# Performance work log

Measured on AMD Instinct MI355X. Metric: run time of the kernel, lower is better.

## Reference

```python
import jax, jax.numpy as jnp
import numpy as np

N, K, D, H, O = 50000, 32, 128, 32, 128


def setup_inputs() -> dict:
    key = jax.random.key(0)
    ks = jax.random.split(key, 8)
    node_feats = jax.random.normal(ks[0], (N, D), dtype=jnp.float32)
    neib_feats = jax.random.normal(ks[1], (N * K, D), dtype=jnp.float32)
    node_ids = jax.random.randint(ks[2], (N,), 0, N)
    neib_ids = jax.random.randint(ks[3], (N * K,), 0, N)
    s = 1.0 / np.sqrt(D)
    W_att1 = jax.random.uniform(ks[4], (D, H), jnp.float32, -s, s)   # Linear(D,H,bias=False)
    sh = 1.0 / np.sqrt(H)
    W_att2 = jax.random.uniform(ks[5], (H, H), jnp.float32, -sh, sh)  # Linear(H,H,bias=False)
    W_node = jax.random.uniform(ks[6], (D, O), jnp.float32, -s, s)
    W_neib = jax.random.uniform(ks[7], (D, O), jnp.float32, -s, s)
    return {"node_feats": node_feats, "neib_feats": neib_feats,
            "node_ids": node_ids, "neib_ids": neib_ids,
            "W_att1": W_att1, "W_att2": W_att2,
            "W_node": W_node, "W_neib": W_neib}


def reference(node_feats, neib_feats, node_ids, neib_ids, W_att1, W_att2, W_node, W_neib):
    n = node_feats.shape[0]
    k = neib_feats.shape[0] // n
    att = lambda x: jnp.tanh(x @ W_att1) @ W_att2           # Linear->Tanh->Linear
    neib_att = att(neib_feats).reshape(n, k, -1)             # [N, K, H]
    node_att = att(node_feats)                               # [N, H]
    scores = jnp.einsum('nkh,nh->nk', neib_att, node_att)    # bmm + squeeze
    ws = jax.nn.softmax(scores, axis=-1)                     # [N, K]
    agg = jnp.einsum('nkd,nk->nd', neib_feats.reshape(n, k, -1), ws)  # weighted neighbor sum
    out = jnp.concatenate([node_feats @ W_node, agg @ W_neib], axis=1)
    return jax.nn.relu(out)
```

## Files before the change

### kernel.cpp

```cpp
#include <hip/hip_runtime.h>

#define N_NODES 50000
#define KNB 32
#define DIM 128
#define HDIM 32

typedef _Float16 f16x8 __attribute__((ext_vector_type(8)));
typedef float f32x16 __attribute__((ext_vector_type(16)));

__device__ __forceinline__ float fast_tanh(float x) {
  float xc = fminf(fmaxf(x, -15.f), 15.f);
  float e = __expf(2.f * xc);
  return (e - 1.f) / (e + 1.f);
}

__global__ __launch_bounds__(256) void k_att(
    const float* __restrict__ node_feats, const float* __restrict__ neib_feats,
    const float* __restrict__ W_att1, const float* __restrict__ W_att2,
    float* __restrict__ out) {
  __shared__ float w2p[HDIM * 33];
  __shared__ float s_tn[4][HDIM];
  __shared__ float s_na[4][HDIM];
  __shared__ float s_sc[4][KNB];

  const int tid = threadIdx.x;
  const int wv = tid >> 6;
  const int l = tid & 63;
  const int lg = l & 31;
  const int hf = l >> 5;

  for (int i = tid; i < HDIM * HDIM; i += 256)
    w2p[(i >> 5) * 33 + (i & 31)] = W_att2[i];

  f16x8 b1[8];
#pragma unroll
  for (int s = 0; s < 8; ++s) {
#pragma unroll
    for (int j = 0; j < 8; ++j) {
      int d = s * 16 + hf * 8 + j;
      b1[s][j] = (_Float16)W_att1[d * HDIM + lg];
    }
  }
  __syncthreads();

  const int waveG = blockIdx.x * 4 + wv;
  const int nW = gridDim.x * 4;
  const int iters = (N_NODES + nW - 1) / nW;

  for (int it = 0; it < iters; ++it) {
    const int n = waveG + it * nW;
    const bool active = n < N_NODES;
    const int nn = active ? n : N_NODES - 1;
    const float* nb = neib_feats + (size_t)nn * (KNB * DIM);
    const float* nd = node_feats + (size_t)nn * DIM;

    f32x16 acc = {0.f, 0.f, 0.f, 0.f, 0.f, 0.f, 0.f, 0.f,
                  0.f, 0.f, 0.f, 0.f, 0.f, 0.f, 0.f, 0.f};
    f32x16 acc2 = {0.f, 0.f, 0.f, 0.f, 0.f, 0.f, 0.f, 0.f,
                   0.f, 0.f, 0.f, 0.f, 0.f, 0.f, 0.f, 0.f};
#pragma unroll
    for (int s = 0; s < 8; ++s) {
      const float* srcA = nb + lg * DIM + s * 16 + hf * 8;
      const float* srcN = nd + s * 16 + hf * 8;
      f16x8 a, an;
#pragma unroll
      for (int j = 0; j < 8; ++j) {
        a[j] = (_Float16)srcA[j];
        an[j] = (_Float16)srcN[j];
      }
      acc = __builtin_amdgcn_mfma_f32_32x32x16_f16(a, b1[s], acc, 0, 0, 0);
      acc2 = __builtin_amdgcn_mfma_f32_32x32x16_f16(an, b1[s], acc2, 0, 0, 0);
    }

    float T[16];
#pragma unroll
    for (int r = 0; r < 16; ++r) T[r] = fast_tanh(acc[r]);

    float tn = fast_tanh(acc2[0]);
    if (l < 32) s_tn[wv][l] = tn;
    __syncthreads();

    float na = 0.f;
#pragma unroll
    for (int g = 0; g < HDIM; ++g) na = fmaf(s_tn[wv][g], w2p[g * 33 + lg], na);
    if (l < 32) s_na[wv][l] = na;
    __syncthreads();

    float v = 0.f;
#pragma unroll
    for (int h = 0; h < HDIM; ++h) v = fmaf(w2p[lg * 33 + h], s_na[wv][h], v);

#pragma unroll
    for (int r = 0; r < 16; ++r) {
      float p = T[r] * v;
#pragma unroll
      for (int off = 1; off <= 16; off <<= 1) p += __shfl_xor(p, off);
      if (lg == 0) s_sc[wv][(r & 3) + 8 * (r >> 2) + 4 * hf] = p;
    }
    __syncthreads();

    float sc = s_sc[wv][lg];
    float mx = sc;
#pragma unroll
    for (int off = 16; off; off >>= 1) mx = fmaxf(mx, __shfl_xor(mx, off));
    float e = __expf(sc - mx);
    float sum = e;
#pragma unroll
    for (int off = 16; off; off >>= 1) sum += __shfl_xor(sum, off);
    float w = e / sum;

    float a0 = 0.f, a1 = 0.f;
#pragma unroll 8
    for (int k = 0; k < KNB; ++k) {
      float wk = __shfl(w, k, 32);
      float2 rv = *(const float2*)(nb + k * DIM + 2 * l);
      a0 = fmaf(wk, rv.x, a0);
      a1 = fmaf(wk, rv.y, a1);
    }
    if (active)
      *(float2*)(out + (size_t)n * 256 + 128 + 2 * l) = make_float2(a0, a1);
  }
}

__global__ __launch_bounds__(256) void k_out(
    const float* __restrict__ node_feats, const float* __restrict__ W_node,
    const float* __restrict__ W_neib, float* __restrict__ out) {
  const int tid = threadIdx.x;
  const int wv = tid >> 6;
  const int l = tid & 63;
  const int lg = l & 31;
  const int hf = l >> 5;
  const int half = blockIdx.y;

  const float* W = half ? W_neib : W_node;
  const int r0 = blockIdx.x * 128 + wv * 32;
  const int row = r0 + lg;
  const int rowc = row < N_NODES ? row : N_NODES - 1;

  const float* X = half ? (out + 128) : node_feats;
  const size_t pitch = half ? 256 : DIM;

  f16x8 a[8];
#pragma unroll
  for (int s = 0; s < 8; ++s) {
    const float* src = X + (size_t)rowc * pitch + s * 16 + hf * 8;
#pragma unroll
    for (int j = 0; j < 8; ++j) a[s][j] = (_Float16)src[j];
  }

  for (int ct = 0; ct < 4; ++ct) {
    f32x16 acc = {0.f, 0.f, 0.f, 0.f, 0.f, 0.f, 0.f, 0.f,
                  0.f, 0.f, 0.f, 0.f, 0.f, 0.f, 0.f, 0.f};
#pragma unroll
    for (int s = 0; s < 8; ++s) {
      f16x8 b;
#pragma unroll
      for (int j = 0; j < 8; ++j) {
        int d = s * 16 + hf * 8 + j;
        b[j] = (_Float16)W[d * 128 + ct * 32 + lg];
      }
      acc = __builtin_amdgcn_mfma_f32_32x32x16_f16(a[s], b, acc, 0, 0, 0);
    }
#pragma unroll
    for (int r = 0; r < 16; ++r) {
      int orow = r0 + (r & 3) + 8 * (r >> 2) + 4 * hf;
      if (orow < N_NODES)
        out[(size_t)orow * 256 + half * 128 + ct * 32 + lg] = fmaxf(acc[r], 0.f);
    }
  }
}

extern "C" void kernel_launch(void* const* d_in, const int* in_sizes, int n_in,
                              void* d_out, int out_size, void* d_ws, size_t ws_size,
                              hipStream_t stream) {
  (void)in_sizes; (void)n_in; (void)d_ws; (void)ws_size; (void)out_size;
  const float* node_feats = (const float*)d_in[0];
  const float* neib_feats = (const float*)d_in[1];
  const float* W_att1 = (const float*)d_in[4];
  const float* W_att2 = (const float*)d_in[5];
  const float* W_node = (const float*)d_in[6];
  const float* W_neib = (const float*)d_in[7];
  float* out = (float*)d_out;

  k_att<<<dim3(768), dim3(256), 0, stream>>>(node_feats, neib_feats, W_att1, W_att2, out);
  k_out<<<dim3((N_NODES + 127) / 128, 2), dim3(256), 0, stream>>>(node_feats, W_node, W_neib, out);
}
```

Before: 1.246 ms.

## Precompute per-node attention query via W2·W2ᵀ and simplify neighbor scoring

After: 1.150 ms. -7.7%, faster.

```diff
diff --git a/kernel.cpp b/kernel.cpp
--- a/kernel.cpp
+++ b/kernel.cpp
@@ -9,105 +9,148 @@
 typedef float f32x16 __attribute__((ext_vector_type(16)));
 
 __device__ __forceinline__ float fast_tanh(float x) {
-  float xc = fminf(fmaxf(x, -15.f), 15.f);
+  float xc = fminf(fmaxf(x, -10.f), 10.f);
   float e = __expf(2.f * xc);
-  return (e - 1.f) / (e + 1.f);
-}
-
-__global__ __launch_bounds__(256) void k_att(
-    const float* __restrict__ node_feats, const float* __restrict__ neib_feats,
-    const float* __restrict__ W_att1, const float* __restrict__ W_att2,
-    float* __restrict__ out) {
-  __shared__ float w2p[HDIM * 33];
-  __shared__ float s_tn[4][HDIM];
-  __shared__ float s_na[4][HDIM];
-  __shared__ float s_sc[4][KNB];
+  return (e - 1.f) * __builtin_amdgcn_rcpf(e + 1.f);
+}
+
+__device__ __forceinline__ f32x16 zero16() {
+  f32x16 z;
+#pragma unroll
+  for (int i = 0; i < 16; ++i) z[i] = 0.f;
+  return z;
+}
+
+__global__ __launch_bounds__(256) void k_node(
+    const float* __restrict__ node_feats, const float* __restrict__ W_att1,
+    const float* __restrict__ W_att2, const float* __restrict__ W_node,
+    float* __restrict__ out, float* __restrict__ v_ws) {
+  __shared__ float w2s[HDIM * HDIM];
+  __shared__ float Ms[HDIM * 33];
+  __shared__ float T2[4][HDIM * 36];
 
   const int tid = threadIdx.x;
-  const int wv = tid >> 6;
-  const int l = tid & 63;
-  const int lg = l & 31;
-  const int hf = l >> 5;
-
-  for (int i = tid; i < HDIM * HDIM; i += 256)
-    w2p[(i >> 5) * 33 + (i & 31)] = W_att2[i];
-
-  f16x8 b1[8];
-#pragma unroll
-  for (int s = 0; s < 8; ++s) {
+  const int wv = tid >> 6, l = tid & 63, lg = l & 31, hf = l >> 5;
+
+  for (int i = tid; i < HDIM * HDIM; i += 256) w2s[i] = W_att2[i];
+  __syncthreads();
+  for (int e = tid; e < HDIM * HDIM; e += 256) {
+    int g = e >> 5, gp = e & 31;
+    float s = 0.f;
+#pragma unroll
+    for (int h = 0; h < HDIM; ++h) s = fmaf(w2s[g * 32 + h], w2s[gp * 32 + h], s);
+    Ms[g * 33 + gp] = s;
+  }
+  __syncthreads();
+
+  const int r0 = blockIdx.x * 128 + wv * 32;
+  const int row = r0 + lg;
+  const int rowc = row < N_NODES ? row : N_NODES - 1;
+
+  f16x8 af[8];
+#pragma unroll
+  for (int s = 0; s < 8; ++s) {
+    const float* src = node_feats + (size_t)rowc * DIM + s * 16 + hf * 8;
+#pragma unroll
+    for (int j = 0; j < 8; ++j) af[s][j] = (_Float16)src[j];
+  }
+
+  f32x16 acc1 = zero16();
+#pragma unroll
+  for (int s = 0; s < 8; ++s) {
+    f16x8 b;
+#pragma unroll
+    for (int j = 0; j < 8; ++j)
+      b[j] = (_Float16)W_att1[(s * 16 + hf * 8 + j) * HDIM + lg];
+    acc1 = __builtin_amdgcn_mfma_f32_32x32x16_f16(af[s], b, acc1, 0, 0, 0);
+  }
+#pragma unroll
+  for (int r = 0; r < 16; ++r)
+    T2[wv][((r & 3) + 8 * (r >> 2) + 4 * hf) * 36 + lg] = fast_tanh(acc1[r]);
+  __syncthreads();
+
+  f32x16 accv = zero16();
+#pragma unroll
+  for (int s = 0; s < 2; ++s) {
+    f16x8 a2, mb;
 #pragma unroll
     for (int j = 0; j < 8; ++j) {
-      int d = s * 16 + hf * 8 + j;
-      b1[s][j] = (_Float16)W_att1[d * HDIM + lg];
-    }
-  }
-  __syncthreads();
+      a2[j] = (_Float16)T2[wv][lg * 36 + s * 16 + hf * 8 + j];
+      mb[j] = (_Float16)Ms[(s * 16 + hf * 8 + j) * 33 + lg];
+    }
+    accv = __builtin_amdgcn_mfma_f32_32x32x16_f16(a2, mb, accv, 0, 0, 0);
+  }
+#pragma unroll
+  for (int r = 0; r < 16; ++r) {
+    int orow = r0 + (r & 3) + 8 * (r >> 2) + 4 * hf;
+    if (orow < N_NODES) v_ws[orow * HDIM + lg] = accv[r];
+  }
+
+  for (int ct = 0; ct < 4; ++ct) {
+    f32x16 acc = zero16();
+#pragma unroll
+    for (int s = 0; s < 8; ++s) {
+      f16x8 b;
+#pragma unroll
+      for (int j = 0; j < 8; ++j)
+        b[j] = (_Float16)W_node[(s * 16 + hf * 8 + j) * 128 + ct * 32 + lg];
+      acc = __builtin_amdgcn_mfma_f32_32x32x16_f16(af[s], b, acc, 0, 0, 0);
+    }
+#pragma unroll
+    for (int r = 0; r < 16; ++r) {
+      int orow = r0 + (r & 3) + 8 * (r >> 2) + 4 * hf;
+      if (orow < N_NODES) out[(size_t)orow * 256 + ct * 32 + lg] = fmaxf(acc[r], 0.f);
+    }
+  }
+}
+
+__global__ __launch_bounds__(256, 3) void k_att(
+    const float* __restrict__ neib_feats, const float* __restrict__ W_att1,
+    const float* __restrict__ v_ws, float* __restrict__ out) {
+  const int tid = threadIdx.x;
+  const int wv = tid >> 6, l = tid & 63, lg = l & 31, hf = l >> 5;
+
+  f16x8 w1t[8];
+#pragma unroll
+  for (int s = 0; s < 8; ++s) {
+#pragma unroll
+    for (int j = 0; j < 8; ++j)
+      w1t[s][j] = (_Float16)W_att1[(s * 16 + hf * 8 + j) * HDIM + lg];
+  }
 
   const int waveG = blockIdx.x * 4 + wv;
   const int nW = gridDim.x * 4;
-  const int iters = (N_NODES + nW - 1) / nW;
-
-  for (int it = 0; it < iters; ++it) {
-    const int n = waveG + it * nW;
-    const bool active = n < N_NODES;
-    const int nn = active ? n : N_NODES - 1;
-    const float* nb = neib_feats + (size_t)nn * (KNB * DIM);
-    const float* nd = node_feats + (size_t)nn * DIM;
-
-    f32x16 acc = {0.f, 0.f, 0.f, 0.f, 0.f, 0.f, 0.f, 0.f,
-                  0.f, 0.f, 0.f, 0.f, 0.f, 0.f, 0.f, 0.f};
-    f32x16 acc2 = {0.f, 0.f, 0.f, 0.f, 0.f, 0.f, 0.f, 0.f,
-                   0.f, 0.f, 0.f, 0.f, 0.f, 0.f, 0.f, 0.f};
+
+  for (int n = waveG; n < N_NODES; n += nW) {
+    const float* nb = neib_feats + (size_t)n * (KNB * DIM);
+
+    f32x16 acc = zero16();
 #pragma unroll
     for (int s = 0; s < 8; ++s) {
-      const float* srcA = nb + lg * DIM + s * 16 + hf * 8;
-      const float* srcN = nd + s * 16 + hf * 8;
-      f16x8 a, an;
-#pragma unroll
-      for (int j = 0; j < 8; ++j) {
-        a[j] = (_Float16)srcA[j];
-        an[j] = (_Float16)srcN[j];
-      }
-      acc = __builtin_amdgcn_mfma_f32_32x32x16_f16(a, b1[s], acc, 0, 0, 0);
-      acc2 = __builtin_amdgcn_mfma_f32_32x32x16_f16(an, b1[s], acc2, 0, 0, 0);
-    }
-
-    float T[16];
-#pragma unroll
-    for (int r = 0; r < 16; ++r) T[r] = fast_tanh(acc[r]);
-
-    float tn = fast_tanh(acc2[0]);
-    if (l < 32) s_tn[wv][l] = tn;
-    __syncthreads();
-
-    float na = 0.f;
-#pragma unroll
-    for (int g = 0; g < HDIM; ++g) na = fmaf(s_tn[wv][g], w2p[g * 33 + lg], na);
-    if (l < 32) s_na[wv][l] = na;
-    __syncthreads();
-
-    float v = 0.f;
-#pragma unroll
-    for (int h = 0; h < HDIM; ++h) v = fmaf(w2p[lg * 33 + h], s_na[wv][h], v);
-
+      const float* src = nb + lg * DIM + s * 16 + hf * 8;
+      f16x8 b;
+#pragma unroll
+      for (int j = 0; j < 8; ++j) b[j] = (_Float16)src[j];
+      acc = __builtin_amdgcn_mfma_f32_32x32x16_f16(w1t[s], b, acc, 0, 0, 0);
+    }
+
+    const float* vn = v_ws + n * HDIM;
+    float p = 0.f;
 #pragma unroll
     for (int r = 0; r < 16; ++r) {
-      float p = T[r] * v;
-#pragma unroll
-      for (int off = 1; off <= 16; off <<= 1) p += __shfl_xor(p, off);
-      if (lg == 0) s_sc[wv][(r & 3) + 8 * (r >> 2) + 4 * hf] = p;
-    }
-    __syncthreads();
-
-    float sc = s_sc[wv][lg];
-    float mx = sc;
-#pragma unroll
-    for (int off = 16; off; off >>= 1) mx = fmaxf(mx, __shfl_xor(mx, off));
-    float e = __expf(sc - mx);
+      float t = fast_tanh(acc[r]);
+      p = fmaf(t, vn[(r & 3) + 8 * (r >> 2) + 4 * hf], p);
+    }
+    p += __shfl_xor(p, 32, 64);
+
+    float mx = p;
+#pragma unroll
+    for (int off = 16; off; off >>= 1) mx = fmaxf(mx, __shfl_xor(mx, off, 32));
+    float e = __expf(p - mx);
     float sum = e;
 #pragma unroll
-    for (int off = 16; off; off >>= 1) sum += __shfl_xor(sum, off);
-    float w = e / sum;
+    for (int off = 16; off; off >>= 1) sum += __shfl_xor(sum, off, 32);
+    float w = e * __builtin_amdgcn_rcpf(sum);
 
     float a0 = 0.f, a1 = 0.f;
 #pragma unroll 8
@@ -117,55 +160,40 @@
       a0 = fmaf(wk, rv.x, a0);
       a1 = fmaf(wk, rv.y, a1);
     }
-    if (active)
-      *(float2*)(out + (size_t)n * 256 + 128 + 2 * l) = make_float2(a0, a1);
-  }
-}
-
-__global__ __launch_bounds__(256) void k_out(
-    const float* __restrict__ node_feats, const float* __restrict__ W_node,
+    *(float2*)(out + (size_t)n * 256 + 128 + 2 * l) = make_float2(a0, a1);
+  }
+}
+
+__global__ __launch_bounds__(256) void k_neib(
     const float* __restrict__ W_neib, float* __restrict__ out) {
   const int tid = threadIdx.x;
-  const int wv = tid >> 6;
-  const int l = tid & 63;
-  const int lg = l & 31;
-  const int hf = l >> 5;
-  const int half = blockIdx.y;
-
-  const float* W = half ? W_neib : W_node;
+  const int wv = tid >> 6, l = tid & 63, lg = l & 31, hf = l >> 5;
   const int r0 = blockIdx.x * 128 + wv * 32;
   const int row = r0 + lg;
   const int rowc = row < N_NODES ? row : N_NODES - 1;
 
-  const float* X = half ? (out + 128) : node_feats;
-  const size_t pitch = half ? 256 : DIM;
-
-  f16x8 a[8];
-#pragma unroll
-  for (int s = 0; s < 8; ++s) {
-    const float* src = X + (size_t)rowc * pitch + s * 16 + hf * 8;
-#pragma unroll
-    for (int j = 0; j < 8; ++j) a[s][j] = (_Float16)src[j];
+  f16x8 af[8];
+#pragma unroll
+  for (int s = 0; s < 8; ++s) {
+    const float* src = out + (size_t)rowc * 256 + 128 + s * 16 + hf * 8;
+#pragma unroll
+    for (int j = 0; j < 8; ++j) af[s][j] = (_Float16)src[j];
   }
 
   for (int ct = 0; ct < 4; ++ct) {
-    f32x16 acc = {0.f, 0.f, 0.f, 0.f, 0.f, 0.f, 0.f, 0.f,
-                  0.f, 0.f, 0.f, 0.f, 0.f, 0.f, 0.f, 0.f};
+    f32x16 acc = zero16();
 #pragma unroll
     for (int s = 0; s < 8; ++s) {
       f16x8 b;
 #pragma unroll
-      for (int j = 0; j < 8; ++j) {
-        int d = s * 16 + hf * 8 + j;
-        b[j] = (_Float16)W[d * 128 + ct * 32 + lg];
-      }
-      acc = __builtin_amdgcn_mfma_f32_32x32x16_f16(a[s], b, acc, 0, 0, 0);
+      for (int j = 0; j < 8; ++j)
+        b[j] = (_Float16)W_neib[(s * 16 + hf * 8 + j) * 128 + ct * 32 + lg];
+      acc = __builtin_amdgcn_mfma_f32_32x32x16_f16(af[s], b, acc, 0, 0, 0);
     }
 #pragma unroll
     for (int r = 0; r < 16; ++r) {
       int orow = r0 + (r & 3) + 8 * (r >> 2) + 4 * hf;
-      if (orow < N_NODES)
-        out[(size_t)orow * 256 + half * 128 + ct * 32 + lg] = fmaxf(acc[r], 0.f);
+      if (orow < N_NODES) out[(size_t)orow * 256 + 128 + ct * 32 + lg] = fmaxf(acc[r], 0.f);
     }
   }
 }
@@ -173,7 +201,7 @@
 extern "C" void kernel_launch(void* const* d_in, const int* in_sizes, int n_in,
                               void* d_out, int out_size, void* d_ws, size_t ws_size,
                               hipStream_t stream) {
-  (void)in_sizes; (void)n_in; (void)d_ws; (void)ws_size; (void)out_size;
+  (void)in_sizes; (void)n_in; (void)ws_size; (void)out_size;
   const float* node_feats = (const float*)d_in[0];
   const float* neib_feats = (const float*)d_in[1];
   const float* W_att1 = (const float*)d_in[4];
@@ -181,7 +209,10 @@
   const float* W_node = (const float*)d_in[6];
   const float* W_neib = (const float*)d_in[7];
   float* out = (float*)d_out;
-
-  k_att<<<dim3(768), dim3(256), 0, stream>>>(node_feats, neib_feats, W_att1, W_att2, out);
-  k_out<<<dim3((N_NODES + 127) / 128, 2), dim3(256), 0, stream>>>(node_feats, W_node, W_neib, out);
-}
+  float* v_ws = (float*)d_ws;
+
+  const int nblk = (N_NODES + 127) / 128;
+  k_node<<<dim3(nblk), dim3(256), 0, stream>>>(node_feats, W_att1, W_att2, W_node, out, v_ws);
+  k_att<<<dim3(1024), dim3(256), 0, stream>>>(neib_feats, W_att1, v_ws, out);
+  k_neib<<<dim3(nblk), dim3(256), 0, stream>>>(W_neib, out);
+}
```
